# Optimization experiments

Hardware: AMD Instinct MI355X
Metric: run time of the kernel (lower is better)

## Reference

```python
import jax, jax.numpy as jnp
import numpy as np

N, C, E, NUM_ID, NUM_LABELS = 50000, 128, 1600000, 2048, 7


def setup_inputs() -> dict:
    key = jax.random.key(0)
    k_x, k_r, k_c, k_id, k_lab, k_w, k_wid = jax.random.split(key, 7)
    x = jax.random.normal(k_x, (N, C), dtype=jnp.float32)
    row = jax.random.randint(k_r, (E,), 0, N)
    col = jax.random.randint(k_c, (E,), 0, N)
    # remove accidental self-loops so the 'add remaining self loops' step
    # (append all N self loops) matches PyG's add_remaining_self_loops exactly
    col = jnp.where(col == row, (col + 1) % N, col)
    edge_index = jnp.stack([row, col]).astype(jnp.int64)
    idx = jax.random.randint(k_id, (NUM_ID,), 0, N).astype(jnp.int64)
    node_label = jax.random.randint(k_lab, (N,), 0, 8).astype(jnp.int64)
    # glorot init
    s = jnp.sqrt(6.0 / (C + C)).astype(jnp.float32)
    weight = jax.random.uniform(k_w, (C, C), minval=-s, maxval=s, dtype=jnp.float32)
    weight_id = jax.random.uniform(k_wid, (NUM_LABELS, C, C), minval=-s, maxval=s, dtype=jnp.float32)
    return {"x": x, "edge_index": edge_index, "id": idx, "node_label": node_label,
            "weight": weight, "weight_id": weight_id}


def reference(x, edge_index, id, node_label, weight, weight_id):
    n = x.shape[0]
    row, col = edge_index[0], edge_index[1]
    # ego-center update: x[id] += x[id] @ W (index_add handles duplicate ids)
    x = x.at[id].add(x[id] @ weight)
    # label-grouped gather-matmul-scatter: ox = x + sum_i mask_i * (x @ W_i)
    ox = x
    for i in range(NUM_LABELS):
        mask = (node_label == i + 1)
        ox = ox + jnp.where(mask[:, None], x @ weight_id[i], jnp.zeros((), x.dtype))
    # GCN symmetric normalization with self loops (fill_value = 1.0)
    loop = jnp.arange(n)
    row_f = jnp.concatenate([row, loop])
    col_f = jnp.concatenate([col, loop])
    ew = jnp.ones((row_f.shape[0],), dtype=x.dtype)
    deg = jax.ops.segment_sum(ew, row_f, num_segments=n)
    dinv = jnp.where(deg > 0, deg ** -0.5, jnp.zeros((), x.dtype))
    norm = dinv[row_f] * ew * dinv[col_f]
    # message = norm * x_j (source row), aggregated by sum at target col
    out = jax.ops.segment_sum(norm[:, None] * ox[row_f], col_f, num_segments=n)
    return out
```

## Files before the change

### kernel.cpp

```cpp
#include <hip/hip_runtime.h>
#include <hip/hip_bf16.h>

typedef unsigned int   u32;
typedef unsigned short u16;
typedef unsigned char  u8;
typedef float f32x2 __attribute__((ext_vector_type(2)));

#define N_NODES 50000
#define C_DIM   128
#define E_EDGES 1600000
#define NUM_IDX 2048

#define CPB 256
#define NB  196
#define CHK 4096
#define NP  391
#define PT  512
#define GB  8

__global__ void label_hist_kernel(const int* __restrict__ label, int* __restrict__ labCnt,
                                  const int* __restrict__ id, int* __restrict__ cnt) {
    __shared__ int h[8];
    if (threadIdx.x < 8) h[threadIdx.x] = 0;
    __syncthreads();
    int n = blockIdx.x * 256 + threadIdx.x;
    if (n < N_NODES) atomicAdd(&h[label[n]], 1);
    if (n < NUM_IDX) atomicAdd(&cnt[id[n]], 1);
    __syncthreads();
    if (threadIdx.x < 8 && h[threadIdx.x] > 0) atomicAdd(&labCnt[threadIdx.x], h[threadIdx.x]);
}

__global__ void chunk_hist_kernel(const int* __restrict__ row, const int* __restrict__ col,
                                  int* __restrict__ Hc, int* __restrict__ Hr) {
    __shared__ int hc[NB], hr[NB];
    int p = blockIdx.x;
    for (int i = threadIdx.x; i < NB; i += PT) { hc[i] = 0; hr[i] = 0; }
    __syncthreads();
    int e0 = p * CHK, e1 = min(e0 + CHK, E_EDGES);
    for (int e = e0 + threadIdx.x; e < e1; e += PT) {
        atomicAdd(&hc[col[e] >> 8], 1);
        atomicAdd(&hr[row[e] >> 8], 1);
    }
    __syncthreads();
    for (int i = threadIdx.x; i < NB; i += PT) {
        Hc[p * NB + i] = hc[i];
        Hr[p * NB + i] = hr[i];
    }
}

__global__ void offsets_kernel(int* __restrict__ Hc, int* __restrict__ Hr,
                               int* __restrict__ colTot, int* __restrict__ rowTot) {
    __shared__ int sc[PT];
    int b = blockIdx.x;
    int j = (b < NB) ? b : b - NB;
    int* H   = (b < NB) ? Hc : Hr;
    int* tot = (b < NB) ? colTot : rowTot;
    int t = threadIdx.x;
    int v = (t < NP) ? H[t * NB + j] : 0;
    sc[t] = v;
    __syncthreads();
    for (int off = 1; off < PT; off <<= 1) {
        int a = (t >= off) ? sc[t - off] : 0;
        int s = sc[t];
        __syncthreads();
        sc[t] = s + a;
        __syncthreads();
    }
    if (t < NP) H[t * NB + j] = sc[t] - v;
    if (t == PT - 1) tot[j] = sc[t];
}

__global__ void bucket_scan_kernel(const int* __restrict__ colTot, const int* __restrict__ rowTot,
                                   int* __restrict__ bucketStart, int* __restrict__ rowStart,
                                   const int* __restrict__ labCnt, int* __restrict__ labCur) {
    __shared__ int sc[256];
    int t = threadIdx.x;
    sc[t] = (t < NB) ? colTot[t] : 0;
    __syncthreads();
    for (int off = 1; off < 256; off <<= 1) {
        int v = sc[t];
        int a = (t >= off) ? sc[t - off] : 0;
        __syncthreads();
        sc[t] = v + a;
        __syncthreads();
    }
    if (t < NB) {
        bucketStart[t] = (t == 0) ? 0 : sc[t - 1];
        if (t == NB - 1) bucketStart[NB] = sc[t];
    }
    __syncthreads();
    sc[t] = (t < NB) ? rowTot[t] : 0;
    __syncthreads();
    for (int off = 1; off < 256; off <<= 1) {
        int v = sc[t];
        int a = (t >= off) ? sc[t - off] : 0;
        __syncthreads();
        sc[t] = v + a;
        __syncthreads();
    }
    if (t < NB) {
        rowStart[t] = (t == 0) ? 0 : sc[t - 1];
        if (t == NB - 1) rowStart[NB] = sc[t];
    }
    if (t == 0) {
        int run = 0;
        for (int i = 0; i < 8; ++i) { labCur[i] = run; run += labCnt[i]; }
    }
}

__global__ void partition_kernel(const int* __restrict__ row, const int* __restrict__ col,
                                 const int* __restrict__ Hc, const int* __restrict__ Hr,
                                 const int* __restrict__ bucketStart, const int* __restrict__ rowStart,
                                 u32* __restrict__ S, u8* __restrict__ Sr) {
    __shared__ int bc_[NB], br_[NB];
    int p = blockIdx.x;
    for (int i = threadIdx.x; i < NB; i += PT) {
        bc_[i] = bucketStart[i] + Hc[p * NB + i];
        br_[i] = rowStart[i]   + Hr[p * NB + i];
    }
    __syncthreads();
    int e0 = p * CHK, e1 = min(e0 + CHK, E_EDGES);
    for (int e = e0 + threadIdx.x; e < e1; e += PT) {
        int r = row[e], c = col[e];
        int pc = atomicAdd(&bc_[c >> 8], 1);
        S[pc] = ((u32)r << 8) | (u32)(c & 255);
        int pr = atomicAdd(&br_[r >> 8], 1);
        Sr[pr] = (u8)(r & 255);
    }
}

__global__ void label_fill_kernel(const int* __restrict__ label, int* __restrict__ labCur,
                                  int* __restrict__ nodeByLabel) {
    __shared__ int h[8], base[8], c2[8];
    int t = threadIdx.x;
    if (t < 8) { h[t] = 0; c2[t] = 0; }
    __syncthreads();
    int n = blockIdx.x * 256 + t;
    int l = 0;
    if (n < N_NODES) { l = label[n]; atomicAdd(&h[l], 1); }
    __syncthreads();
    if (t < 8 && h[t] > 0) base[t] = atomicAdd(&labCur[t], h[t]);
    __syncthreads();
    if (n < N_NODES) {
        int pos = base[l] + atomicAdd(&c2[l], 1);
        nodeByLabel[pos] = n;
    }
}

__global__ void csr_deg_kernel(const u32* __restrict__ S, const u8* __restrict__ Sr,
                               const int* __restrict__ bucketStart, const int* __restrict__ rowStart,
                               int* __restrict__ start, u16* __restrict__ srcrow,
                               float* __restrict__ dinv) {
    __shared__ int h[CPB], cur[CPB], sc[CPB];
    int t = threadIdx.x;
    if (blockIdx.x >= NB) {
        int b = blockIdx.x - NB;
        if (t < CPB) h[t] = 0;
        __syncthreads();
        int e0 = rowStart[b], e1 = rowStart[b + 1];
        for (int e = e0 + t; e < e1; e += PT) atomicAdd(&h[Sr[e]], 1);
        __syncthreads();
        if (t < CPB) {
            int n = b * CPB + t;
            if (n < N_NODES) dinv[n] = rsqrtf((float)(h[t] + 1));
        }
        return;
    }
    int b = blockIdx.x;
    if (t < CPB) h[t] = 0;
    __syncthreads();
    int e0 = bucketStart[b], e1 = bucketStart[b + 1];
    for (int e = e0 + t; e < e1; e += PT) atomicAdd(&h[S[e] & 255u], 1);
    __syncthreads();
    if (t < CPB) sc[t] = h[t];
    __syncthreads();
    for (int off = 1; off < CPB; off <<= 1) {
        int v = 0, a = 0;
        if (t < CPB) { v = sc[t]; a = (t >= off) ? sc[t - off] : 0; }
        __syncthreads();
        if (t < CPB) sc[t] = v + a;
        __syncthreads();
    }
    if (t < CPB) {
        int base = (t == 0) ? 0 : sc[t - 1];
        int gcol = b * CPB + t;
        if (gcol < N_NODES) start[gcol] = e0 + base;
        cur[t] = base;
    }
    if (b == NB - 1 && t == 0) start[N_NODES] = E_EDGES;
    __syncthreads();
    for (int e = e0 + t; e < e1; e += PT) {
        u32 v = S[e];
        int pos = atomicAdd(&cur[v & 255u], 1);
        srcrow[e0 + pos] = (u16)(v >> 8);
    }
}

__global__ void node_msg_kernel(const float* __restrict__ x,
                                const int* __restrict__ cnt,
                                const int* __restrict__ label,
                                const float* __restrict__ dinv,
                                const float* __restrict__ W,
                                const float* __restrict__ Wid,
                                const int* __restrict__ nodeByLabel,
                                __hip_bfloat16* __restrict__ msgb) {
    __shared__ float xs[GB][C_DIM];
    __shared__ int nid[GB], lab[GB], cc[GB];
    int t = threadIdx.x;
    if (t < GB) {
        int n = nodeByLabel[blockIdx.x * GB + t];
        nid[t] = n; lab[t] = label[n]; cc[t] = cnt[n];
    }
    __syncthreads();
    #pragma unroll
    for (int g = 0; g < GB; ++g)
        xs[g][t] = __builtin_nontemporal_load(x + (size_t)nid[g] * C_DIM + t);
    __syncthreads();
    for (int g = 0; g < GB; ++g) {
        int c = cc[g];
        if (c > 0) {
            float acc = 0.f;
            #pragma unroll 8
            for (int k = 0; k < C_DIM; ++k) acc += xs[g][k] * W[k * C_DIM + t];
            __syncthreads();
            xs[g][t] += (float)c * acc;
            __syncthreads();
        }
    }
    float res[GB];
    #pragma unroll
    for (int g = 0; g < GB; ++g) res[g] = xs[g][t];
    if (lab[0] == lab[GB - 1]) {
        int L = lab[0];
        if (L > 0) {
            const float* Wl = Wid + (size_t)(L - 1) * C_DIM * C_DIM;
            float acc[GB];
            #pragma unroll
            for (int g = 0; g < GB; ++g) acc[g] = 0.f;
            for (int k = 0; k < C_DIM; ++k) {
                float w = Wl[k * C_DIM + t];
                #pragma unroll
                for (int g = 0; g < GB; ++g) acc[g] += xs[g][k] * w;
            }
            #pragma unroll
            for (int g = 0; g < GB; ++g) res[g] += acc[g];
        }
    } else {
        for (int g = 0; g < GB; ++g) {
            int L = lab[g];
            if (L > 0) {
                const float* Wl = Wid + (size_t)(L - 1) * C_DIM * C_DIM;
                float acc = 0.f;
                #pragma unroll 8
                for (int k = 0; k < C_DIM; ++k) acc += xs[g][k] * Wl[k * C_DIM + t];
                res[g] += acc;
            }
        }
    }
    #pragma unroll
    for (int g = 0; g < GB; ++g) {
        int n = nid[g];
        msgb[(size_t)n * C_DIM + t] = __float2bfloat16(dinv[n] * res[g]);
    }
}

__global__ void gather_kernel(const int* __restrict__ start,
                              const u16* __restrict__ srcrow,
                              const float* __restrict__ dinv,
                              const u32* __restrict__ m32,
                              float* __restrict__ out) {
    int wid  = threadIdx.x >> 6;
    int lane = threadIdx.x & 63;
    int c = blockIdx.x * 4 + wid;
    int e0 = start[c], e1 = start[c + 1];
    u32 u = m32[((u32)c << 6) | lane];
    float a0 = __uint_as_float(u << 16);
    float a1 = __uint_as_float(u & 0xffff0000u);
    int e = e0;
    for (; e + 8 <= e1; e += 8) {
        u32 rr[8], uu[8];
        #pragma unroll
        for (int j = 0; j < 8; ++j) rr[j] = srcrow[e + j];
        #pragma unroll
        for (int j = 0; j < 8; ++j) uu[j] = m32[(rr[j] << 6) | (u32)lane];
        #pragma unroll
        for (int j = 0; j < 8; ++j) {
            a0 += __uint_as_float(uu[j] << 16);
            a1 += __uint_as_float(uu[j] & 0xffff0000u);
        }
    }
    for (; e < e1; ++e) {
        u32 ue = m32[((u32)srcrow[e] << 6) | (u32)lane];
        a0 += __uint_as_float(ue << 16);
        a1 += __uint_as_float(ue & 0xffff0000u);
    }
    float di = dinv[c];
    f32x2 o; o.x = di * a0; o.y = di * a1;
    __builtin_nontemporal_store(o, (f32x2*)out + (((u32)c << 6) | lane));
}

extern "C" void kernel_launch(void* const* d_in, const int* in_sizes, int n_in,
                              void* d_out, int out_size, void* d_ws, size_t ws_size,
                              hipStream_t stream) {
    const float* x     = (const float*)d_in[0];
    const int*   edge  = (const int*)d_in[1];
    const int*   id    = (const int*)d_in[2];
    const int*   label = (const int*)d_in[3];
    const float* W     = (const float*)d_in[4];
    const float* Wid   = (const float*)d_in[5];
    float*       out   = (float*)d_out;

    const int* row = edge;
    const int* col = edge + E_EDGES;

    __hip_bfloat16* msgb = (__hip_bfloat16*)d_ws;
    u32* S           = (u32*)(msgb + (size_t)N_NODES * C_DIM);
    u16* srcrow      = (u16*)(S + E_EDGES);
    u8*  Sr          = (u8*)(srcrow + E_EDGES);
    int* start       = (int*)(Sr + E_EDGES);
    int* bucketStart = start + (N_NODES + 1);
    int* rowStart    = bucketStart + (NB + 1);
    int* Hc          = rowStart + (NB + 1);
    int* Hr          = Hc + NP * NB;
    int* colTot      = Hr + NP * NB;
    int* rowTot      = colTot + NB;
    int* nodeByLabel = rowTot + NB;
    float* dinv      = (float*)(nodeByLabel + N_NODES);
    int* cnt         = (int*)(dinv + N_NODES);
    int* labCnt      = cnt + N_NODES;
    int* labCur      = labCnt + 8;

    hipMemsetAsync(cnt, 0, ((size_t)N_NODES + 16) * sizeof(int), stream);

    label_hist_kernel <<<196, 256, 0, stream>>>(label, labCnt, id, cnt);
    chunk_hist_kernel <<<NP, PT, 0, stream>>>(row, col, Hc, Hr);
    offsets_kernel    <<<2 * NB, PT, 0, stream>>>(Hc, Hr, colTot, rowTot);
    bucket_scan_kernel<<<1, 256, 0, stream>>>(colTot, rowTot, bucketStart, rowStart,
                                              labCnt, labCur);
    partition_kernel  <<<NP, PT, 0, stream>>>(row, col, Hc, Hr, bucketStart, rowStart, S, Sr);
    label_fill_kernel <<<196, 256, 0, stream>>>(label, labCur, nodeByLabel);
    csr_deg_kernel    <<<2 * NB, PT, 0, stream>>>(S, Sr, bucketStart, rowStart,
                                                  start, srcrow, dinv);
    node_msg_kernel   <<<N_NODES / GB, C_DIM, 0, stream>>>(x, cnt, label, dinv, W, Wid,
                                                           nodeByLabel, msgb);
    gather_kernel     <<<N_NODES / 4, 256, 0, stream>>>(start, srcrow, dinv,
                                                        (const u32*)msgb, out);
}
```

Baseline: 241.1 us.

## Merge label histogram/fill into edge hist/partition kernels and enlarge node_msg group

Folds the label histogram and id-count work into the edge chunk-histogram launch as extra blocks, and folds the label-based node bucketing into the partition launch, removing two kernel launches and their serialization gaps. It also raises GB from 8 to 16, so node_msg_kernel processes more nodes per block with half as many blocks. The larger GB changes per-block work and parallelism in the matmul kernel, which could help through weight reuse or hurt occupancy.

```diff
diff --git a/kernel.cpp b/kernel.cpp
--- a/kernel.cpp
+++ b/kernel.cpp
@@ -16,40 +16,45 @@
 #define CHK 4096
 #define NP  391
 #define PT  512
-#define GB  8
-
-__global__ void label_hist_kernel(const int* __restrict__ label, int* __restrict__ labCnt,
-                                  const int* __restrict__ id, int* __restrict__ cnt) {
-    __shared__ int h[8];
-    if (threadIdx.x < 8) h[threadIdx.x] = 0;
-    __syncthreads();
-    int n = blockIdx.x * 256 + threadIdx.x;
-    if (n < N_NODES) atomicAdd(&h[label[n]], 1);
-    if (n < NUM_IDX) atomicAdd(&cnt[id[n]], 1);
-    __syncthreads();
-    if (threadIdx.x < 8 && h[threadIdx.x] > 0) atomicAdd(&labCnt[threadIdx.x], h[threadIdx.x]);
-}
-
-__global__ void chunk_hist_kernel(const int* __restrict__ row, const int* __restrict__ col,
-                                  int* __restrict__ Hc, int* __restrict__ Hr) {
+#define NLB 98
+#define GB  16
+
+__global__ __launch_bounds__(PT) void hist_all_kernel(
+        const int* __restrict__ row, const int* __restrict__ col,
+        int* __restrict__ Hc, int* __restrict__ Hr,
+        const int* __restrict__ label, int* __restrict__ labCnt,
+        const int* __restrict__ id, int* __restrict__ cnt) {
+    int t = threadIdx.x;
+    if (blockIdx.x >= NP) {
+        __shared__ int h[8];
+        if (t < 8) h[t] = 0;
+        __syncthreads();
+        int n = (blockIdx.x - NP) * PT + t;
+        if (n < N_NODES) atomicAdd(&h[label[n]], 1);
+        if (n < NUM_IDX) atomicAdd(&cnt[id[n]], 1);
+        __syncthreads();
+        if (t < 8 && h[t] > 0) atomicAdd(&labCnt[t], h[t]);
+        return;
+    }
     __shared__ int hc[NB], hr[NB];
     int p = blockIdx.x;
-    for (int i = threadIdx.x; i < NB; i += PT) { hc[i] = 0; hr[i] = 0; }
+    for (int i = t; i < NB; i += PT) { hc[i] = 0; hr[i] = 0; }
     __syncthreads();
     int e0 = p * CHK, e1 = min(e0 + CHK, E_EDGES);
-    for (int e = e0 + threadIdx.x; e < e1; e += PT) {
+    for (int e = e0 + t; e < e1; e += PT) {
         atomicAdd(&hc[col[e] >> 8], 1);
         atomicAdd(&hr[row[e] >> 8], 1);
     }
     __syncthreads();
-    for (int i = threadIdx.x; i < NB; i += PT) {
+    for (int i = t; i < NB; i += PT) {
         Hc[p * NB + i] = hc[i];
         Hr[p * NB + i] = hr[i];
     }
 }
 
-__global__ void offsets_kernel(int* __restrict__ Hc, int* __restrict__ Hr,
-                               int* __restrict__ colTot, int* __restrict__ rowTot) {
+__global__ __launch_bounds__(PT) void offsets_kernel(
+        int* __restrict__ Hc, int* __restrict__ Hr,
+        int* __restrict__ colTot, int* __restrict__ rowTot) {
     __shared__ int sc[PT];
     int b = blockIdx.x;
     int j = (b < NB) ? b : b - NB;
@@ -108,19 +113,39 @@
     }
 }
 
-__global__ void partition_kernel(const int* __restrict__ row, const int* __restrict__ col,
-                                 const int* __restrict__ Hc, const int* __restrict__ Hr,
-                                 const int* __restrict__ bucketStart, const int* __restrict__ rowStart,
-                                 u32* __restrict__ S, u8* __restrict__ Sr) {
+__global__ __launch_bounds__(PT) void part_fill_kernel(
+        const int* __restrict__ row, const int* __restrict__ col,
+        const int* __restrict__ Hc, const int* __restrict__ Hr,
+        const int* __restrict__ bucketStart, const int* __restrict__ rowStart,
+        u32* __restrict__ S, u8* __restrict__ Sr,
+        const int* __restrict__ label, int* __restrict__ labCur,
+        int* __restrict__ nodeByLabel) {
+    int t = threadIdx.x;
+    if (blockIdx.x >= NP) {
+        __shared__ int h8[8], base8[8], c28[8];
+        if (t < 8) { h8[t] = 0; c28[t] = 0; }
+        __syncthreads();
+        int n = (blockIdx.x - NP) * PT + t;
+        int l = 0;
+        if (n < N_NODES) { l = label[n]; atomicAdd(&h8[l], 1); }
+        __syncthreads();
+        if (t < 8 && h8[t] > 0) base8[t] = atomicAdd(&labCur[t], h8[t]);
+        __syncthreads();
+        if (n < N_NODES) {
+            int pos = base8[l] + atomicAdd(&c28[l], 1);
+            nodeByLabel[pos] = n;
+        }
+        return;
+    }
     __shared__ int bc_[NB], br_[NB];
     int p = blockIdx.x;
-    for (int i = threadIdx.x; i < NB; i += PT) {
+    for (int i = t; i < NB; i += PT) {
         bc_[i] = bucketStart[i] + Hc[p * NB + i];
         br_[i] = rowStart[i]   + Hr[p * NB + i];
     }
     __syncthreads();
     int e0 = p * CHK, e1 = min(e0 + CHK, E_EDGES);
-    for (int e = e0 + threadIdx.x; e < e1; e += PT) {
+    for (int e = e0 + t; e < e1; e += PT) {
         int r = row[e], c = col[e];
         int pc = atomicAdd(&bc_[c >> 8], 1);
         S[pc] = ((u32)r << 8) | (u32)(c & 255);
@@ -129,28 +154,11 @@
     }
 }
 
-__global__ void label_fill_kernel(const int* __restrict__ label, int* __restrict__ labCur,
-                                  int* __restrict__ nodeByLabel) {
-    __shared__ int h[8], base[8], c2[8];
-    int t = threadIdx.x;
-    if (t < 8) { h[t] = 0; c2[t] = 0; }
-    __syncthreads();
-    int n = blockIdx.x * 256 + t;
-    int l = 0;
-    if (n < N_NODES) { l = label[n]; atomicAdd(&h[l], 1); }
-    __syncthreads();
-    if (t < 8 && h[t] > 0) base[t] = atomicAdd(&labCur[t], h[t]);
-    __syncthreads();
-    if (n < N_NODES) {
-        int pos = base[l] + atomicAdd(&c2[l], 1);
-        nodeByLabel[pos] = n;
-    }
-}
-
-__global__ void csr_deg_kernel(const u32* __restrict__ S, const u8* __restrict__ Sr,
-                               const int* __restrict__ bucketStart, const int* __restrict__ rowStart,
-                               int* __restrict__ start, u16* __restrict__ srcrow,
-                               float* __restrict__ dinv) {
+__global__ __launch_bounds__(PT) void csr_deg_kernel(
+        const u32* __restrict__ S, const u8* __restrict__ Sr,
+        const int* __restrict__ bucketStart, const int* __restrict__ rowStart,
+        int* __restrict__ start, u16* __restrict__ srcrow,
+        float* __restrict__ dinv) {
     __shared__ int h[CPB], cur[CPB], sc[CPB];
     int t = threadIdx.x;
     if (blockIdx.x >= NB) {
@@ -332,13 +340,13 @@
 
     hipMemsetAsync(cnt, 0, ((size_t)N_NODES + 16) * sizeof(int), stream);
 
-    label_hist_kernel <<<196, 256, 0, stream>>>(label, labCnt, id, cnt);
-    chunk_hist_kernel <<<NP, PT, 0, stream>>>(row, col, Hc, Hr);
+    hist_all_kernel   <<<NP + NLB, PT, 0, stream>>>(row, col, Hc, Hr,
+                                                    label, labCnt, id, cnt);
     offsets_kernel    <<<2 * NB, PT, 0, stream>>>(Hc, Hr, colTot, rowTot);
     bucket_scan_kernel<<<1, 256, 0, stream>>>(colTot, rowTot, bucketStart, rowStart,
                                               labCnt, labCur);
-    partition_kernel  <<<NP, PT, 0, stream>>>(row, col, Hc, Hr, bucketStart, rowStart, S, Sr);
-    label_fill_kernel <<<196, 256, 0, stream>>>(label, labCur, nodeByLabel);
+    part_fill_kernel  <<<NP + NLB, PT, 0, stream>>>(row, col, Hc, Hr, bucketStart, rowStart,
+                                                    S, Sr, label, labCur, nodeByLabel);
     csr_deg_kernel    <<<2 * NB, PT, 0, stream>>>(S, Sr, bucketStart, rowStart,
                                                   start, srcrow, dinv);
     node_msg_kernel   <<<N_NODES / GB, C_DIM, 0, stream>>>(x, cnt, label, dinv, W, Wid,
```

New measurement: 252.4 us. 1.05x slower.
